# Performance work log

Hardware: AMD Instinct MI355X
Metric: run time of the kernel (lower is better)

The kernel has to match this reference:

```python
import jax, jax.numpy as jnp
import numpy as np

PAD = 0
BOS = 101
D = 768
H = 12
DH = D // H
DFF = 3072
V = 30522


def _ln(x, eps=1e-5):
    m = jnp.mean(x, axis=-1, keepdims=True)
    v = jnp.var(x, axis=-1, keepdims=True)
    return (x - m) * jax.lax.rsqrt(v + eps)


def setup_inputs() -> dict:
    key = jax.random.key(0)
    ks = jax.random.split(key, 20)
    B, S = 8, 128
    s = 0.02
    p = lambda k, sh: (jax.random.normal(k, sh, dtype=jnp.float32) * s)
    inp = {
        "X": jax.random.randint(ks[0], (B, S), 0, V, dtype=jnp.int32),
        "emb": p(ks[1], (V, D)),
        "pos": p(ks[2], (512, D)),
        "Wq": p(ks[3], (D, D)), "Wk": p(ks[4], (D, D)),
        "Wv": p(ks[5], (D, D)), "Wo": p(ks[6], (D, D)),
        "W1": p(ks[7], (D, DFF)), "W2": p(ks[8], (DFF, D)),
        "Wdq": p(ks[9], (D, D)), "Wdk": p(ks[10], (D, D)),
        "Wdv": p(ks[11], (D, D)), "Wdo": p(ks[12], (D, D)),
        "Wd1": p(ks[13], (D, DFF)), "Wd2": p(ks[14], (DFF, D)),
        "Wvoc": p(ks[15], (D, V)),
        "max_tgt_len": 32,
        "beam_width": 4,
    }
    return inp


def reference(X, emb, pos, Wq, Wk, Wv, Wo, W1, W2,
              Wdq, Wdk, Wdv, Wdo, Wd1, Wd2, Wvoc,
              max_tgt_len, beam_width):
    B, S = X.shape
    K = beam_width
    T = max_tgt_len
    scale = 1.0 / np.sqrt(DH)

    # ---- BERT-style encoder (1 layer) ----
    src_mask = (X != PAD)                              # [B,S]
    mb = jnp.where(src_mask, 0.0, -1e9)[:, None, None, :]  # [B,1,1,S]
    h = emb[X] + pos[:S][None]                         # [B,S,D]
    q = (h @ Wq).reshape(B, S, H, DH)
    k = (h @ Wk).reshape(B, S, H, DH)
    v = (h @ Wv).reshape(B, S, H, DH)
    att = jax.nn.softmax(jnp.einsum('bqhd,bkhd->bhqk', q, k) * scale + mb, axis=-1)
    ctx = jnp.einsum('bhqk,bkhd->bqhd', att, v).reshape(B, S, D) @ Wo
    h = _ln(h + ctx)
    h = _ln(h + jax.nn.gelu(h @ W1) @ W2)
    memory = h                                         # [B,S,D]

    # precompute cross-attn K/V once
    Kmem = (memory @ Wdk).reshape(B, S, H, DH)
    Vmem = (memory @ Wdv).reshape(B, S, H, DH)

    # ---- beam search decode ----
    tokens0 = jnp.full((B, K), BOS, dtype=jnp.int32)
    scores0 = jnp.broadcast_to(
        jnp.concatenate([jnp.zeros((1,)), jnp.full((K - 1,), -1e9)]).astype(jnp.float32),
        (B, K))

    def step(carry, t):
        tokens, scores = carry                         # [B,K], [B,K]
        x = emb[tokens] + pos[t][None, None]           # [B,K,D]
        qd = (x @ Wdq).reshape(B, K, H, DH)
        a = jax.nn.softmax(
            jnp.einsum('bkhd,bshd->bhks', qd, Kmem) * scale + mb, axis=-1)
        c = jnp.einsum('bhks,bshd->bkhd', a, Vmem).reshape(B, K, D) @ Wdo
        hd = _ln(x + c)
        hd = _ln(hd + jax.nn.gelu(hd @ Wd1) @ Wd2)
        logp = jax.nn.log_softmax(hd @ Wvoc, axis=-1)  # [B,K,V]
        total = (scores[:, :, None] + logp).reshape(B, K * V)
        new_scores, idx = jax.lax.top_k(total, K)      # [B,K]
        beam_idx = (idx // V).astype(jnp.int32)
        tok = (idx % V).astype(jnp.int32)
        return (tok, new_scores), (beam_idx, tok)

    (toksT, scoresT), (beam_hist, tok_hist) = jax.lax.scan(
        step, (tokens0, scores0), jnp.arange(T))

    # ---- backtrack through back-pointers ----
    ptr0 = jnp.broadcast_to(jnp.arange(K, dtype=jnp.int32), (B, K))

    def back(ptr, bt):
        beam_idx, tok = bt                             # [B,K] each
        seq_t = jnp.take_along_axis(tok, ptr, axis=1)
        ptr = jnp.take_along_axis(beam_idx, ptr, axis=1)
        return ptr, seq_t

    _, seq = jax.lax.scan(back, ptr0, (beam_hist, tok_hist), reverse=True)
    seq = jnp.transpose(seq, (1, 2, 0))                # [B,K,T]
    return seq, scoresT
```

## Files before the change

kernel.cpp:

```cpp
#include <hip/hip_runtime.h>
#include <math.h>

#define DMODEL 768
#define HN 12
#define DHEAD 64
#define DFF 3072
#define VOC 30522
#define BB 8
#define SS 128
#define KW 4
#define TT 32
#define CHN 239

__device__ __forceinline__ float gelu_f(float x) {
    float x3 = x * x * x;
    return 0.5f * x * (1.0f + tanhf(0.7978845608028654f * (x + 0.044715f * x3)));
}

__global__ void init_k(int* tokens, float* scores) {
    int i = threadIdx.x;
    if (i < BB * KW) {
        tokens[i] = 101;
        scores[i] = (i & 3) ? -1e9f : 0.0f;
    }
}

__global__ __launch_bounds__(256) void embed_enc(const int* __restrict__ X,
                                                 const float* __restrict__ emb,
                                                 const float* __restrict__ pos,
                                                 float* __restrict__ h,
                                                 float* __restrict__ mb) {
    int row = blockIdx.x;
    int s = row & (SS - 1);
    int tok = X[row];
    const float* e = emb + (size_t)tok * DMODEL;
    const float* p = pos + (size_t)s * DMODEL;
    float* hp = h + (size_t)row * DMODEL;
    for (int c = threadIdx.x; c < DMODEL; c += 256) hp[c] = e[c] + p[c];
    if (threadIdx.x == 0) mb[row] = (tok != 0) ? 0.0f : -1e9f;
}

template<int KD, int ACT>
__global__ __launch_bounds__(256) void gemm64(const float* __restrict__ A,
                                              const float* __restrict__ B,
                                              float* __restrict__ C, int N) {
    __shared__ float As[16][68];
    __shared__ float Bs[16][68];
    int tid = threadIdx.x;
    int tx = tid & 15, ty = tid >> 4;
    int bm = blockIdx.y * 64, bn = blockIdx.x * 64;
    int a_gk = tid & 15, a_gm0 = tid >> 4;
    int b_gn = tid & 63, b_gk0 = tid >> 6;
    float ra[4], rb[4];
    float acc[4][4] = {};
#pragma unroll
    for (int p = 0; p < 4; p++) ra[p] = A[(size_t)(bm + a_gm0 + p * 16) * KD + a_gk];
#pragma unroll
    for (int p = 0; p < 4; p++) rb[p] = B[(size_t)(b_gk0 + p * 4) * N + bn + b_gn];
    for (int k0 = 0; k0 < KD; k0 += 16) {
        __syncthreads();
#pragma unroll
        for (int p = 0; p < 4; p++) As[a_gk][a_gm0 + p * 16] = ra[p];
#pragma unroll
        for (int p = 0; p < 4; p++) Bs[b_gk0 + p * 4][b_gn] = rb[p];
        __syncthreads();
        if (k0 + 16 < KD) {
#pragma unroll
            for (int p = 0; p < 4; p++) ra[p] = A[(size_t)(bm + a_gm0 + p * 16) * KD + k0 + 16 + a_gk];
#pragma unroll
            for (int p = 0; p < 4; p++) rb[p] = B[(size_t)(k0 + 16 + b_gk0 + p * 4) * N + bn + b_gn];
        }
#pragma unroll
        for (int kk = 0; kk < 16; kk++) {
            float4 a4 = *(const float4*)&As[kk][ty * 4];
            float4 b4 = *(const float4*)&Bs[kk][tx * 4];
            float av[4] = {a4.x, a4.y, a4.z, a4.w};
            float bv[4] = {b4.x, b4.y, b4.z, b4.w};
#pragma unroll
            for (int i = 0; i < 4; i++)
#pragma unroll
                for (int j = 0; j < 4; j++) acc[i][j] += av[i] * bv[j];
        }
    }
#pragma unroll
    for (int i = 0; i < 4; i++)
#pragma unroll
        for (int j = 0; j < 4; j++) {
            float v = acc[i][j];
            if (ACT) v = gelu_f(v);
            C[(size_t)(bm + ty * 4 + i) * N + bn + tx * 4 + j] = v;
        }
}

__global__ __launch_bounds__(64) void enc_attn(const float* __restrict__ q,
                                               const float* __restrict__ k,
                                               const float* __restrict__ v,
                                               const float* __restrict__ mb,
                                               float* __restrict__ ctx) {
    int bid = blockIdx.x;
    int qi = bid & (SS - 1);
    int h = (bid >> 7) % HN;
    int b = bid / (SS * HN);
    int lane = threadIdx.x;
    __shared__ float qs[DHEAD];
    __shared__ float att[SS];
    qs[lane] = q[((size_t)(b * SS + qi) * HN + h) * DHEAD + lane];
    __syncthreads();
    const float* kb = k + ((size_t)(b * SS) * HN + h) * DHEAD;
    const float* k0p = kb + (size_t)lane * DMODEL;
    const float* k1p = kb + (size_t)(lane + 64) * DMODEL;
    float s0 = 0.f, s1 = 0.f;
#pragma unroll 8
    for (int d = 0; d < DHEAD; d++) {
        float qd = qs[d];
        s0 += qd * k0p[d];
        s1 += qd * k1p[d];
    }
    s0 = s0 * 0.125f + mb[b * SS + lane];
    s1 = s1 * 0.125f + mb[b * SS + lane + 64];
    float m = fmaxf(s0, s1);
    for (int off = 32; off; off >>= 1) m = fmaxf(m, __shfl_xor(m, off, 64));
    float e0 = expf(s0 - m), e1 = expf(s1 - m);
    float sum = e0 + e1;
    for (int off = 32; off; off >>= 1) sum += __shfl_xor(sum, off, 64);
    float inv = 1.0f / sum;
    att[lane] = e0 * inv;
    att[lane + 64] = e1 * inv;
    __syncthreads();
    const float* vb = v + ((size_t)(b * SS) * HN + h) * DHEAD + lane;
    float acc = 0.f;
#pragma unroll 8
    for (int key = 0; key < SS; key++) acc += att[key] * vb[(size_t)key * DMODEL];
    ctx[(size_t)(b * SS + qi) * DMODEL + h * DHEAD + lane] = acc;
}

template<int P>
__global__ __launch_bounds__(256) void lnresP(const float* __restrict__ A,
                                              const float* __restrict__ Bsrc,
                                              float* __restrict__ out,
                                              float* __restrict__ outT,
                                              int wantT, int planeStride) {
    int row = blockIdx.x, tid = threadIdx.x;
    const float* ap = A + (size_t)row * DMODEL;
    float x[3];
#pragma unroll
    for (int i = 0; i < 3; i++) {
        int idx = tid + 256 * i;
        float s = ap[idx];
#pragma unroll
        for (int p = 0; p < P; p++) s += Bsrc[(size_t)p * planeStride + (size_t)row * DMODEL + idx];
        x[i] = s;
    }
    __shared__ float red[256];
    __shared__ float sm, sv;
    red[tid] = x[0] + x[1] + x[2];
    __syncthreads();
    for (int off = 128; off; off >>= 1) { if (tid < off) red[tid] += red[tid + off]; __syncthreads(); }
    if (tid == 0) sm = red[0] * (1.0f / DMODEL);
    __syncthreads();
    float mean = sm;
    float d[3], s2 = 0.f;
#pragma unroll
    for (int i = 0; i < 3; i++) { d[i] = x[i] - mean; s2 += d[i] * d[i]; }
    __syncthreads();
    red[tid] = s2;
    __syncthreads();
    for (int off = 128; off; off >>= 1) { if (tid < off) red[tid] += red[tid + off]; __syncthreads(); }
    if (tid == 0) sv = 1.0f / sqrtf(red[0] * (1.0f / DMODEL) + 1e-5f);
    __syncthreads();
    float inv = sv;
    float* op = out + (size_t)row * DMODEL;
#pragma unroll
    for (int i = 0; i < 3; i++) {
        float val = d[i] * inv;
        op[tid + 256 * i] = val;
        if (wantT) outT[(size_t)(tid + 256 * i) * 32 + row] = val;
    }
}

__global__ __launch_bounds__(256) void embed_dec(const int* __restrict__ tokens,
                                                 const float* __restrict__ emb,
                                                 const float* __restrict__ pos,
                                                 int t, float* __restrict__ x,
                                                 float* __restrict__ xT) {
    int row = blockIdx.x;
    int tok = tokens[row];
    const float* e = emb + (size_t)tok * DMODEL;
    const float* p = pos + (size_t)t * DMODEL;
    for (int c = threadIdx.x; c < DMODEL; c += 256) {
        float v = e[c] + p[c];
        x[(size_t)row * DMODEL + c] = v;
        xT[(size_t)c * 32 + row] = v;
    }
}

template<int KRANGE, int APL, int AGELU, int TOUT>
__global__ __launch_bounds__(256) void skinny3(const float* __restrict__ At,
                                               const float* __restrict__ B,
                                               float* __restrict__ C,
                                               int N, int aPlaneF4) {
    constexpr int SK = (KRANGE > 192) ? 192 : KRANGE;
    constexpr int NST = KRANGE / SK;
    __shared__ float Als[SK * 32];
    int tid = threadIdx.x;
    int lane = tid & 63, q = tid >> 6;
    int col0 = blockIdx.x * 128 + lane * 2;
    float acc[8][2] = {};
    for (int st = 0; st < NST; st++) {
        int kbase = blockIdx.y * KRANGE + st * SK;
        __syncthreads();
        const float4* srcb = ((const float4*)At) + (size_t)kbase * 8;
        float4* dst = (float4*)Als;
#pragma unroll
        for (int i = 0; i < SK / 32; i++) {
            float4 v = srcb[i * 256 + tid];
#pragma unroll
            for (int p = 1; p < APL; p++) {
                float4 w = srcb[(size_t)p * aPlaneF4 + i * 256 + tid];
                v.x += w.x; v.y += w.y; v.z += w.z; v.w += w.w;
            }
            if (AGELU) { v.x = gelu_f(v.x); v.y = gelu_f(v.y); v.z = gelu_f(v.z); v.w = gelu_f(v.w); }
            dst[i * 256 + tid] = v;
        }
        __syncthreads();
        const float* Bp = B + (size_t)kbase * N + col0;
#pragma unroll 8
        for (int k = 0; k < SK; k++) {
            float2 bv = *(const float2*)(Bp + (size_t)k * N);
            float4 a0 = *(const float4*)&Als[k * 32 + q * 8];
            float4 a1 = *(const float4*)&Als[k * 32 + q * 8 + 4];
            float ar[8] = {a0.x, a0.y, a0.z, a0.w, a1.x, a1.y, a1.z, a1.w};
#pragma unroll
            for (int r = 0; r < 8; r++) {
                acc[r][0] += ar[r] * bv.x;
                acc[r][1] += ar[r] * bv.y;
            }
        }
    }
    float* Cb = C + (size_t)blockIdx.y * 32 * N;
    if (TOUT) {
#pragma unroll
        for (int c = 0; c < 2; c++) {
            float4 lo = {acc[0][c], acc[1][c], acc[2][c], acc[3][c]};
            float4 hi = {acc[4][c], acc[5][c], acc[6][c], acc[7][c]};
            *(float4*)&Cb[(size_t)(col0 + c) * 32 + q * 8] = lo;
            *(float4*)&Cb[(size_t)(col0 + c) * 32 + q * 8 + 4] = hi;
        }
    } else {
#pragma unroll
        for (int r = 0; r < 8; r++) {
            float2 st2 = {acc[r][0], acc[r][1]};
            *(float2*)&Cb[(size_t)(q * 8 + r) * N + col0] = st2;
        }
    }
}

__global__ __launch_bounds__(64) void dec_attn(const float* __restrict__ qdp,
                                               const float* __restrict__ Kmem,
                                               const float* __restrict__ Vmem,
                                               const float* __restrict__ mb,
                                               float* __restrict__ cctxT) {
    const int QP = 32 * DMODEL;
    int bid = blockIdx.x;
    int h = bid % HN;
    int kb = (bid / HN) & 3;
    int b = bid / (HN * KW);
    int lane = threadIdx.x;
    int rowq = b * KW + kb;
    __shared__ float qs[DHEAD];
    __shared__ float att[SS];
    size_t qoff = (size_t)rowq * DMODEL + h * DHEAD + lane;
    float qv = 0.f;
#pragma unroll
    for (int p = 0; p < 8; p++) qv += qdp[(size_t)p * QP + qoff];
    qs[lane] = qv;
    __syncthreads();
    const float* kb0 = Kmem + ((size_t)(b * SS) * HN + h) * DHEAD;
    const float* k0p = kb0 + (size_t)lane * DMODEL;
    const float* k1p = kb0 + (size_t)(lane + 64) * DMODEL;
    float s0 = 0.f, s1 = 0.f;
#pragma unroll 8
    for (int d = 0; d < DHEAD; d++) {
        float qd = qs[d];
        s0 += qd * k0p[d];
        s1 += qd * k1p[d];
    }
    s0 = s0 * 0.125f + mb[b * SS + lane];
    s1 = s1 * 0.125f + mb[b * SS + lane + 64];
    float m = fmaxf(s0, s1);
    for (int off = 32; off; off >>= 1) m = fmaxf(m, __shfl_xor(m, off, 64));
    float e0 = expf(s0 - m), e1 = expf(s1 - m);
    float sum = e0 + e1;
    for (int off = 32; off; off >>= 1) sum += __shfl_xor(sum, off, 64);
    float inv = 1.0f / sum;
    att[lane] = e0 * inv;
    att[lane + 64] = e1 * inv;
    __syncthreads();
    const float* vb = Vmem + ((size_t)(b * SS) * HN + h) * DHEAD + lane;
    float acc = 0.f;
#pragma unroll 8
    for (int key = 0; key < SS; key++) acc += att[key] * vb[(size_t)key * DMODEL];
    cctxT[(size_t)(h * DHEAD + lane) * 32 + rowq] = acc;
}

__global__ __launch_bounds__(256) void logits_stats(const float* __restrict__ At,
                                                    const float* __restrict__ B,
                                                    float* __restrict__ cmax,
                                                    float* __restrict__ csum,
                                                    float* __restrict__ ctv,
                                                    int* __restrict__ cti) {
    __shared__ float Als[192 * 32];
    int tid = threadIdx.x;
    int lane = tid & 63, q = tid >> 6;
    int col0 = blockIdx.x * 128 + lane * 2;
    bool valid = col0 < VOC;
    int jc = valid ? col0 : VOC - 2;
    float acc[8][2] = {};
    for (int st = 0; st < 4; st++) {
        int kbase = st * 192;
        __syncthreads();
        const float4* srcb = ((const float4*)At) + (size_t)kbase * 8;
        float4* dst = (float4*)Als;
#pragma unroll
        for (int i = 0; i < 6; i++) dst[i * 256 + tid] = srcb[i * 256 + tid];
        __syncthreads();
        const float* Bp = B + (size_t)kbase * VOC + jc;
#pragma unroll 8
        for (int k = 0; k < 192; k++) {
            float2 bv = *(const float2*)(Bp + (size_t)k * VOC);
            float4 a0 = *(const float4*)&Als[k * 32 + q * 8];
            float4 a1 = *(const float4*)&Als[k * 32 + q * 8 + 4];
            float ar[8] = {a0.x, a0.y, a0.z, a0.w, a1.x, a1.y, a1.z, a1.w};
#pragma unroll
            for (int r = 0; r < 8; r++) {
                acc[r][0] += ar[r] * bv.x;
                acc[r][1] += ar[r] * bv.y;
            }
        }
    }
#pragma unroll 1
    for (int r = 0; r < 8; r++) {
        float v0 = valid ? acc[r][0] : -INFINITY;
        float v1 = valid ? acc[r][1] : -INFINITY;
        float mx = fmaxf(v0, v1);
#pragma unroll
        for (int off = 32; off; off >>= 1) mx = fmaxf(mx, __shfl_xor(mx, off, 64));
        float ss = valid ? (expf(v0 - mx) + expf(v1 - mx)) : 0.0f;
#pragma unroll
        for (int off = 32; off; off >>= 1) ss += __shfl_xor(ss, off, 64);
        float c0 = v0, c1 = v1;
        int i0 = col0, i1 = col0 + 1;
        float tv[4]; int ti[4];
#pragma unroll
        for (int p = 0; p < 4; p++) {
            float bv; int bi;
            if (c0 > c1 || (c0 == c1 && i0 < i1)) { bv = c0; bi = i0; } else { bv = c1; bi = i1; }
#pragma unroll
            for (int off = 32; off; off >>= 1) {
                float ov = __shfl_xor(bv, off, 64);
                int oi = __shfl_xor(bi, off, 64);
                if (ov > bv || (ov == bv && oi < bi)) { bv = ov; bi = oi; }
            }
            if (bi == i0) c0 = -INFINITY;
            else if (bi == i1) c1 = -INFINITY;
            tv[p] = bv; ti[p] = bi;
        }
        if (lane == 0) {
            int m = q * 8 + r;
            int o = m * CHN + blockIdx.x;
            cmax[o] = mx; csum[o] = ss;
            ctv[o * 4 + 0] = tv[0]; cti[o * 4 + 0] = ti[0];
            ctv[o * 4 + 1] = tv[1]; cti[o * 4 + 1] = ti[1];
            ctv[o * 4 + 2] = tv[2]; cti[o * 4 + 2] = ti[2];
            ctv[o * 4 + 3] = tv[3]; cti[o * 4 + 3] = ti[3];
        }
    }
}

__global__ __launch_bounds__(256) void merge_topk(const float* __restrict__ cmax,
                                                  const float* __restrict__ csum,
                                                  const float* __restrict__ ctv,
                                                  const int* __restrict__ cti,
                                                  float* scores, int* tokens,
                                                  int* beamh, int* tokh, int t) {
    int b = blockIdx.x, tid = threadIdx.x;
    int lane = tid & 63, q = tid >> 6;
    int m = b * 4 + q;
    __shared__ float LSE[4], s_old[4];
    __shared__ float bt_v[4][4];
    __shared__ int bt_i[4][4];
    if (tid < 4) s_old[tid] = scores[b * 4 + tid];
    float mx = -INFINITY, sm = 0.f;
    for (int c = lane; c < CHN; c += 64) {
        float cm = cmax[m * CHN + c], cs = csum[m * CHN + c];
        if (cm > mx) { sm = sm * expf(mx - cm) + cs; mx = cm; }
        else sm += cs * expf(cm - mx);
    }
#pragma unroll
    for (int off = 32; off; off >>= 1) {
        float om = __shfl_xor(mx, off, 64);
        float os = __shfl_xor(sm, off, 64);
        float M = fmaxf(mx, om);
        sm = sm * expf(mx - M) + os * expf(om - M);
        mx = M;
    }
    if (lane == 0) LSE[q] = mx + logf(sm);
    float lv[4] = {-INFINITY, -INFINITY, -INFINITY, -INFINITY};
    int li[4] = {0x7fffffff, 0x7fffffff, 0x7fffffff, 0x7fffffff};
    for (int c = lane; c < CHN; c += 64) {
        int o = (m * CHN + c) * 4;
#pragma unroll
        for (int j = 0; j < 4; j++) {
            float v = ctv[o + j]; int i = cti[o + j];
            if (v > lv[3] || (v == lv[3] && i < li[3])) {
                lv[3] = v; li[3] = i;
#pragma unroll
                for (int s = 3; s > 0; s--) {
                    if (lv[s] > lv[s - 1] || (lv[s] == lv[s - 1] && li[s] < li[s - 1])) {
                        float tv2 = lv[s]; lv[s] = lv[s - 1]; lv[s - 1] = tv2;
                        int ti2 = li[s]; li[s] = li[s - 1]; li[s - 1] = ti2;
                    }
                }
            }
        }
    }
#pragma unroll
    for (int p = 0; p < 4; p++) {
        float bv = lv[0]; int bi = li[0];
#pragma unroll
        for (int off = 32; off; off >>= 1) {
            float ov = __shfl_xor(bv, off, 64);
            int oi = __shfl_xor(bi, off, 64);
            if (ov > bv || (ov == bv && oi < bi)) { bv = ov; bi = oi; }
        }
        if (li[0] == bi) {
            lv[0] = lv[1]; li[0] = li[1];
            lv[1] = lv[2]; li[1] = li[2];
            lv[2] = lv[3]; li[2] = li[3];
            lv[3] = -INFINITY; li[3] = 0x7fffffff;
        }
        if (lane == 0) { bt_v[q][p] = bv; bt_i[q][p] = bi; }
    }
    __syncthreads();
    if (tid == 0) {
        float fv[16]; int fi[16]; bool used[16];
#pragma unroll
        for (int r = 0; r < 4; r++)
#pragma unroll
            for (int p = 0; p < 4; p++) {
                fv[r * 4 + p] = s_old[r] - LSE[r] + bt_v[r][p];
                fi[r * 4 + p] = r * VOC + bt_i[r][p];
                used[r * 4 + p] = false;
            }
        for (int kk = 0; kk < 4; kk++) {
            int best = -1;
            for (int c2 = 0; c2 < 16; c2++) {
                if (used[c2]) continue;
                if (best < 0 || fv[c2] > fv[best] || (fv[c2] == fv[best] && fi[c2] < fi[best])) best = c2;
            }
            used[best] = true;
            int beam = fi[best] / VOC;
            int tok = fi[best] - beam * VOC;
            scores[b * 4 + kk] = fv[best];
            tokens[b * 4 + kk] = tok;
            beamh[(t * BB + b) * 4 + kk] = beam;
            tokh[(t * BB + b) * 4 + kk] = tok;
        }
    }
}

__global__ void backtrack_k(const int* __restrict__ beamh, const int* __restrict__ tokh,
                            const float* __restrict__ scores, float* __restrict__ out) {
    int i = threadIdx.x;
    if (i < BB * KW) {
        int b = i >> 2, k = i & 3;
        int ptr = k;
        for (int t = TT - 1; t >= 0; t--) {
            int tok = tokh[(t * BB + b) * KW + ptr];
            out[(size_t)i * TT + t] = (float)tok;
            ptr = beamh[(t * BB + b) * KW + ptr];
        }
        out[BB * KW * TT + i] = scores[i];
    }
}

extern "C" void kernel_launch(void* const* d_in, const int* in_sizes, int n_in,
                              void* d_out, int out_size, void* d_ws, size_t ws_size,
                              hipStream_t stream) {
    const int* X = (const int*)d_in[0];
    const float* emb = (const float*)d_in[1];
    const float* pos = (const float*)d_in[2];
    const float* Wq = (const float*)d_in[3];
    const float* Wk = (const float*)d_in[4];
    const float* Wv = (const float*)d_in[5];
    const float* Wo = (const float*)d_in[6];
    const float* W1 = (const float*)d_in[7];
    const float* W2 = (const float*)d_in[8];
    const float* Wdq = (const float*)d_in[9];
    const float* Wdk = (const float*)d_in[10];
    const float* Wdv = (const float*)d_in[11];
    const float* Wdo = (const float*)d_in[12];
    const float* Wd1 = (const float*)d_in[13];
    const float* Wd2 = (const float*)d_in[14];
    const float* Wvoc = (const float*)d_in[15];

    float* ws = (float*)d_ws;
    size_t o = 0;
    auto alloc = [&](size_t n) { float* p = ws + o; o += n; return p; };

    const size_t ROWS = (size_t)BB * SS;
    const size_t HD = ROWS * DMODEL;
    const size_t P32 = 32 * DMODEL;

    float* mb = alloc(ROWS);
    float* Kmem = alloc(HD);
    float* Vmem = alloc(HD);
    float* scores = alloc(32);
    int* tokens = (int*)alloc(32);
    int* beamh = (int*)alloc(TT * BB * KW);
    int* tokh = (int*)alloc(TT * BB * KW);

    size_t mark = o;
    float* h0 = alloc(HD);
    float* qb = alloc(HD);
    float* kb = alloc(HD);
    float* vb = alloc(HD);
    float* attc = alloc(HD);
    float* attp = alloc(HD);
    float* h1 = alloc(HD);
    float* ff1 = alloc(ROWS * DFF);
    float* ff2 = alloc(HD);
    float* memb = alloc(HD);

    o = mark;
    float* x = alloc(P32);
    float* xT = alloc(P32);
    float* qdp = alloc(8 * P32);
    float* cctxT = alloc(P32);
    float* cprojp = alloc(8 * P32);
    float* hd1 = alloc(P32);
    float* hd1T = alloc(P32);
    float* dff1p = alloc((size_t)4 * DFF * 32);
    float* dff2p = alloc(8 * P32);
    float* hd2 = alloc(P32);
    float* hd2T = alloc(P32);
    float* cmax = alloc(32 * CHN);
    float* csum = alloc(32 * CHN);
    float* ctv = alloc((size_t)32 * CHN * 4);
    int* cti = (int*)alloc((size_t)32 * CHN * 4);
    (void)ws_size; (void)in_sizes; (void)n_in; (void)out_size;

    init_k<<<1, 64, 0, stream>>>(tokens, scores);

    embed_enc<<<dim3(ROWS), 256, 0, stream>>>(X, emb, pos, h0, mb);
    dim3 g768(DMODEL / 64, ROWS / 64);
    dim3 g3072(DFF / 64, ROWS / 64);
    gemm64<DMODEL, 0><<<g768, 256, 0, stream>>>(h0, Wq, qb, DMODEL);
    gemm64<DMODEL, 0><<<g768, 256, 0, stream>>>(h0, Wk, kb, DMODEL);
    gemm64<DMODEL, 0><<<g768, 256, 0, stream>>>(h0, Wv, vb, DMODEL);
    enc_attn<<<dim3(BB * HN * SS), 64, 0, stream>>>(qb, kb, vb, mb, attc);
    gemm64<DMODEL, 0><<<g768, 256, 0, stream>>>(attc, Wo, attp, DMODEL);
    lnresP<1><<<dim3(ROWS), 256, 0, stream>>>(h0, attp, h1, nullptr, 0, 0);
    gemm64<DMODEL, 1><<<g3072, 256, 0, stream>>>(h1, W1, ff1, DFF);
    gemm64<DFF, 0><<<g768, 256, 0, stream>>>(ff1, W2, ff2, DMODEL);
    lnresP<1><<<dim3(ROWS), 256, 0, stream>>>(h1, ff2, memb, nullptr, 0, 0);
    gemm64<DMODEL, 0><<<g768, 256, 0, stream>>>(memb, Wdk, Kmem, DMODEL);
    gemm64<DMODEL, 0><<<g768, 256, 0, stream>>>(memb, Wdv, Vmem, DMODEL);

    for (int t = 0; t < TT; t++) {
        embed_dec<<<dim3(32), 256, 0, stream>>>(tokens, emb, pos, t, x, xT);
        skinny3<96, 1, 0, 0><<<dim3(6, 8), 256, 0, stream>>>(xT, Wdq, qdp, DMODEL, 0);
        dec_attn<<<dim3(BB * KW * HN), 64, 0, stream>>>(qdp, Kmem, Vmem, mb, cctxT);
        skinny3<96, 1, 0, 0><<<dim3(6, 8), 256, 0, stream>>>(cctxT, Wdo, cprojp, DMODEL, 0);
        lnresP<8><<<dim3(32), 256, 0, stream>>>(x, cprojp, hd1, hd1T, 1, (int)P32);
        skinny3<192, 1, 0, 1><<<dim3(24, 4), 256, 0, stream>>>(hd1T, Wd1, dff1p, DFF, 0);
        skinny3<384, 4, 1, 0><<<dim3(6, 8), 256, 0, stream>>>(dff1p, Wd2, dff2p, DMODEL, DFF * 8);
        lnresP<8><<<dim3(32), 256, 0, stream>>>(hd1, dff2p, hd2, hd2T, 1, (int)P32);
        logits_stats<<<dim3(CHN), 256, 0, stream>>>(hd2T, Wvoc, cmax, csum, ctv, cti);
        merge_topk<<<dim3(BB), 256, 0, stream>>>(cmax, csum, ctv, cti,
                                                 scores, tokens, beamh, tokh, t);
    }

    backtrack_k<<<1, 64, 0, stream>>>(beamh, tokh, scores, (float*)d_out);
}
```

Baseline: 9.355 ms.

## Fuse beam-search decode loop into a persistent kernel with grid barriers

Replaces the 320+ per-step kernel launches of the decode loop with one persistent kernel of 256 blocks. Each stage becomes a device function, and an atomic grid-wide barrier separates the stages. This removes launch overhead and inter-kernel gaps, at the cost of every block spinning at each barrier and all stages sharing one block configuration. The logits inner loop unroll factor is also raised, and initialization and backtracking move into the persistent kernel. The design relies on all 256 blocks being co-resident, or the barrier deadlocks.

Result: slower. 24.88 ms (+166.0%).

```diff
diff --git a/kernel.cpp b/kernel.cpp
--- a/kernel.cpp
+++ b/kernel.cpp
@@ -11,19 +11,14 @@
 #define KW 4
 #define TT 32
 #define CHN 239
+#define PG 256
+#define P32C (32 * DMODEL)
 
 __device__ __forceinline__ float gelu_f(float x) {
     float x3 = x * x * x;
     return 0.5f * x * (1.0f + tanhf(0.7978845608028654f * (x + 0.044715f * x3)));
 }
 
-__global__ void init_k(int* tokens, float* scores) {
-    int i = threadIdx.x;
-    if (i < BB * KW) {
-        tokens[i] = 101;
-        scores[i] = (i & 3) ? -1e9f : 0.0f;
-    }
-}
 
 __global__ __launch_bounds__(256) void embed_enc(const int* __restrict__ X,
                                                  const float* __restrict__ emb,
@@ -178,12 +173,30 @@
     }
 }
 
-__global__ __launch_bounds__(256) void embed_dec(const int* __restrict__ tokens,
-                                                 const float* __restrict__ emb,
-                                                 const float* __restrict__ pos,
-                                                 int t, float* __restrict__ x,
-                                                 float* __restrict__ xT) {
-    int row = blockIdx.x;
+
+__device__ __forceinline__ void gsync(unsigned* bar) {
+    __syncthreads();
+    if (threadIdx.x == 0) {
+        __threadfence();
+        unsigned g0 = __hip_atomic_load(bar + 1, __ATOMIC_RELAXED, __HIP_MEMORY_SCOPE_AGENT);
+        unsigned a = __hip_atomic_fetch_add(bar, 1u, __ATOMIC_ACQ_REL, __HIP_MEMORY_SCOPE_AGENT);
+        if (a == PG - 1) {
+            __hip_atomic_store(bar, 0u, __ATOMIC_RELAXED, __HIP_MEMORY_SCOPE_AGENT);
+            __hip_atomic_fetch_add(bar + 1, 1u, __ATOMIC_RELEASE, __HIP_MEMORY_SCOPE_AGENT);
+        } else {
+            while (__hip_atomic_load(bar + 1, __ATOMIC_RELAXED, __HIP_MEMORY_SCOPE_AGENT) == g0)
+                __builtin_amdgcn_s_sleep(2);
+        }
+        __threadfence();
+    }
+    __syncthreads();
+}
+
+__device__ __forceinline__ void embed_body(const int* __restrict__ tokens,
+                                           const float* __restrict__ emb,
+                                           const float* __restrict__ pos,
+                                           int t, float* __restrict__ x,
+                                           float* __restrict__ xT, int row) {
     int tok = tokens[row];
     const float* e = emb + (size_t)tok * DMODEL;
     const float* p = pos + (size_t)t * DMODEL;
@@ -195,19 +208,19 @@
 }
 
 template<int KRANGE, int APL, int AGELU, int TOUT>
-__global__ __launch_bounds__(256) void skinny3(const float* __restrict__ At,
-                                               const float* __restrict__ B,
-                                               float* __restrict__ C,
-                                               int N, int aPlaneF4) {
+__device__ __forceinline__ void skinny3_body(float* Als,
+                                             const float* __restrict__ At,
+                                             const float* __restrict__ B,
+                                             float* __restrict__ C,
+                                             int N, int aPlaneF4, int bx, int by) {
     constexpr int SK = (KRANGE > 192) ? 192 : KRANGE;
     constexpr int NST = KRANGE / SK;
-    __shared__ float Als[SK * 32];
     int tid = threadIdx.x;
     int lane = tid & 63, q = tid >> 6;
-    int col0 = blockIdx.x * 128 + lane * 2;
+    int col0 = bx * 128 + lane * 2;
     float acc[8][2] = {};
     for (int st = 0; st < NST; st++) {
-        int kbase = blockIdx.y * KRANGE + st * SK;
+        int kbase = by * KRANGE + st * SK;
         __syncthreads();
         const float4* srcb = ((const float4*)At) + (size_t)kbase * 8;
         float4* dst = (float4*)Als;
@@ -237,7 +250,7 @@
             }
         }
     }
-    float* Cb = C + (size_t)blockIdx.y * 32 * N;
+    float* Cb = C + (size_t)by * 32 * N;
     if (TOUT) {
 #pragma unroll
         for (int c = 0; c < 2; c++) {
@@ -255,20 +268,22 @@
     }
 }
 
-__global__ __launch_bounds__(64) void dec_attn(const float* __restrict__ qdp,
-                                               const float* __restrict__ Kmem,
-                                               const float* __restrict__ Vmem,
-                                               const float* __restrict__ mb,
-                                               float* __restrict__ cctxT) {
+__device__ __forceinline__ void dec_attn_body(float* smem,
+                                              const float* __restrict__ qdp,
+                                              const float* __restrict__ Kmem,
+                                              const float* __restrict__ Vmem,
+                                              const float* __restrict__ mb,
+                                              float* __restrict__ cctxT, int vb) {
     const int QP = 32 * DMODEL;
-    int bid = blockIdx.x;
-    int h = bid % HN;
-    int kb = (bid / HN) & 3;
-    int b = bid / (HN * KW);
-    int lane = threadIdx.x;
+    int tid = threadIdx.x;
+    int w = tid >> 6, lane = tid & 63;
+    int unit = vb * 4 + w;
+    int h = unit % HN;
+    int kb = (unit / HN) & 3;
+    int b = unit / (HN * KW);
     int rowq = b * KW + kb;
-    __shared__ float qs[DHEAD];
-    __shared__ float att[SS];
+    float* qs = smem + w * 64;
+    float* att = smem + 256 + w * SS;
     size_t qoff = (size_t)rowq * DMODEL + h * DHEAD + lane;
     float qv = 0.f;
 #pragma unroll
@@ -296,23 +311,67 @@
     att[lane] = e0 * inv;
     att[lane + 64] = e1 * inv;
     __syncthreads();
-    const float* vb = Vmem + ((size_t)(b * SS) * HN + h) * DHEAD + lane;
+    const float* vb2 = Vmem + ((size_t)(b * SS) * HN + h) * DHEAD + lane;
     float acc = 0.f;
 #pragma unroll 8
-    for (int key = 0; key < SS; key++) acc += att[key] * vb[(size_t)key * DMODEL];
+    for (int key = 0; key < SS; key++) acc += att[key] * vb2[(size_t)key * DMODEL];
     cctxT[(size_t)(h * DHEAD + lane) * 32 + rowq] = acc;
 }
 
-__global__ __launch_bounds__(256) void logits_stats(const float* __restrict__ At,
-                                                    const float* __restrict__ B,
-                                                    float* __restrict__ cmax,
-                                                    float* __restrict__ csum,
-                                                    float* __restrict__ ctv,
-                                                    int* __restrict__ cti) {
-    __shared__ float Als[192 * 32];
+template<int P>
+__device__ __forceinline__ void lnres_body(float* smem,
+                                           const float* __restrict__ A,
+                                           const float* __restrict__ Bsrc,
+                                           float* __restrict__ out,
+                                           float* __restrict__ outT,
+                                           int planeStride, int row) {
+    int tid = threadIdx.x;
+    const float* ap = A + (size_t)row * DMODEL;
+    float xx[3];
+#pragma unroll
+    for (int i = 0; i < 3; i++) {
+        int idx = tid + 256 * i;
+        float s = ap[idx];
+#pragma unroll
+        for (int p = 0; p < P; p++) s += Bsrc[(size_t)p * planeStride + (size_t)row * DMODEL + idx];
+        xx[i] = s;
+    }
+    float* red = smem;
+    red[tid] = xx[0] + xx[1] + xx[2];
+    __syncthreads();
+    for (int off = 128; off; off >>= 1) { if (tid < off) red[tid] += red[tid + off]; __syncthreads(); }
+    if (tid == 0) smem[256] = red[0] * (1.0f / DMODEL);
+    __syncthreads();
+    float mean = smem[256];
+    float d[3], s2 = 0.f;
+#pragma unroll
+    for (int i = 0; i < 3; i++) { d[i] = xx[i] - mean; s2 += d[i] * d[i]; }
+    __syncthreads();
+    red[tid] = s2;
+    __syncthreads();
+    for (int off = 128; off; off >>= 1) { if (tid < off) red[tid] += red[tid + off]; __syncthreads(); }
+    if (tid == 0) smem[257] = 1.0f / sqrtf(red[0] * (1.0f / DMODEL) + 1e-5f);
+    __syncthreads();
+    float inv = smem[257];
+    float* op = out + (size_t)row * DMODEL;
+#pragma unroll
+    for (int i = 0; i < 3; i++) {
+        float val = d[i] * inv;
+        op[tid + 256 * i] = val;
+        outT[(size_t)(tid + 256 * i) * 32 + row] = val;
+    }
+}
+
+__device__ __forceinline__ void logits_body(float* Als,
+                                            const float* __restrict__ At,
+                                            const float* __restrict__ B,
+                                            float* __restrict__ cmax,
+                                            float* __restrict__ csum,
+                                            float* __restrict__ ctv,
+                                            int* __restrict__ cti, int bx) {
     int tid = threadIdx.x;
     int lane = tid & 63, q = tid >> 6;
-    int col0 = blockIdx.x * 128 + lane * 2;
+    int col0 = bx * 128 + lane * 2;
     bool valid = col0 < VOC;
     int jc = valid ? col0 : VOC - 2;
     float acc[8][2] = {};
@@ -325,7 +384,7 @@
         for (int i = 0; i < 6; i++) dst[i * 256 + tid] = srcb[i * 256 + tid];
         __syncthreads();
         const float* Bp = B + (size_t)kbase * VOC + jc;
-#pragma unroll 8
+#pragma unroll 16
         for (int k = 0; k < 192; k++) {
             float2 bv = *(const float2*)(Bp + (size_t)k * VOC);
             float4 a0 = *(const float4*)&Als[k * 32 + q * 8];
@@ -367,7 +426,7 @@
         }
         if (lane == 0) {
             int m = q * 8 + r;
-            int o = m * CHN + blockIdx.x;
+            int o = m * CHN + bx;
             cmax[o] = mx; csum[o] = ss;
             ctv[o * 4 + 0] = tv[0]; cti[o * 4 + 0] = ti[0];
             ctv[o * 4 + 1] = tv[1]; cti[o * 4 + 1] = ti[1];
@@ -377,18 +436,22 @@
     }
 }
 
-__global__ __launch_bounds__(256) void merge_topk(const float* __restrict__ cmax,
-                                                  const float* __restrict__ csum,
-                                                  const float* __restrict__ ctv,
-                                                  const int* __restrict__ cti,
-                                                  float* scores, int* tokens,
-                                                  int* beamh, int* tokh, int t) {
-    int b = blockIdx.x, tid = threadIdx.x;
+__device__ __forceinline__ void merge_body(float* smem,
+                                           const float* __restrict__ cmax,
+                                           const float* __restrict__ csum,
+                                           const float* __restrict__ ctv,
+                                           const int* __restrict__ cti,
+                                           float* __restrict__ scores,
+                                           int* __restrict__ tokens,
+                                           int* __restrict__ beamh,
+                                           int* __restrict__ tokh, int t, int b) {
+    int tid = threadIdx.x;
     int lane = tid & 63, q = tid >> 6;
     int m = b * 4 + q;
-    __shared__ float LSE[4], s_old[4];
-    __shared__ float bt_v[4][4];
-    __shared__ int bt_i[4][4];
+    float* s_old = smem;
+    float* LSE = smem + 4;
+    float* bt_v = smem + 8;
+    int* bt_i = (int*)(smem + 24);
     if (tid < 4) s_old[tid] = scores[b * 4 + tid];
     float mx = -INFINITY, sm = 0.f;
     for (int c = lane; c < CHN; c += 64) {
@@ -439,7 +502,7 @@
             lv[2] = lv[3]; li[2] = li[3];
             lv[3] = -INFINITY; li[3] = 0x7fffffff;
         }
-        if (lane == 0) { bt_v[q][p] = bv; bt_i[q][p] = bi; }
+        if (lane == 0) { bt_v[q * 4 + p] = bv; bt_i[q * 4 + p] = bi; }
     }
     __syncthreads();
     if (tid == 0) {
@@ -448,8 +511,8 @@
         for (int r = 0; r < 4; r++)
 #pragma unroll
             for (int p = 0; p < 4; p++) {
-                fv[r * 4 + p] = s_old[r] - LSE[r] + bt_v[r][p];
-                fi[r * 4 + p] = r * VOC + bt_i[r][p];
+                fv[r * 4 + p] = s_old[r] - LSE[r] + bt_v[r * 4 + p];
+                fi[r * 4 + p] = r * VOC + bt_i[r * 4 + p];
                 used[r * 4 + p] = false;
             }
         for (int kk = 0; kk < 4; kk++) {
@@ -469,19 +532,69 @@
     }
 }
 
-__global__ void backtrack_k(const int* __restrict__ beamh, const int* __restrict__ tokh,
-                            const float* __restrict__ scores, float* __restrict__ out) {
-    int i = threadIdx.x;
-    if (i < BB * KW) {
-        int b = i >> 2, k = i & 3;
+__global__ __launch_bounds__(256) void decode_persistent(
+    const float* __restrict__ emb, const float* __restrict__ pos,
+    const float* __restrict__ Wdq, const float* __restrict__ Wdo,
+    const float* __restrict__ Wd1, const float* __restrict__ Wd2,
+    const float* __restrict__ Wvoc,
+    const float* __restrict__ Kmem, const float* __restrict__ Vmem,
+    const float* __restrict__ mb,
+    float* __restrict__ x, float* __restrict__ xT,
+    float* __restrict__ qdp, float* __restrict__ cctxT, float* __restrict__ cprojp,
+    float* __restrict__ hd1, float* __restrict__ hd1T,
+    float* __restrict__ dff1p, float* __restrict__ dff2p,
+    float* __restrict__ hd2, float* __restrict__ hd2T,
+    float* __restrict__ cmax, float* __restrict__ csum,
+    float* __restrict__ ctv, int* __restrict__ cti,
+    float* __restrict__ scores, int* __restrict__ tokens,
+    int* __restrict__ beamh, int* __restrict__ tokh,
+    unsigned* bar, float* __restrict__ out) {
+    __shared__ float smem[6160];
+    int bid = blockIdx.x, tid = threadIdx.x;
+
+    if (bid == 0 && tid < BB * KW) {
+        tokens[tid] = 101;
+        scores[tid] = (tid & 3) ? -1e9f : 0.0f;
+    }
+    gsync(bar);
+
+    for (int t = 0; t < TT; t++) {
+        if (bid < 32) embed_body(tokens, emb, pos, t, x, xT, bid);
+        gsync(bar);
+        if (bid < 48) skinny3_body<96, 1, 0, 0>(smem, xT, Wdq, qdp, DMODEL, 0, bid % 6, bid / 6);
+        gsync(bar);
+        if (bid < 96) dec_attn_body(smem, qdp, Kmem, Vmem, mb, cctxT, bid);
+        gsync(bar);
+        if (bid < 48) skinny3_body<96, 1, 0, 0>(smem, cctxT, Wdo, cprojp, DMODEL, 0, bid % 6, bid / 6);
+        gsync(bar);
+        if (bid < 32) lnres_body<8>(smem, x, cprojp, hd1, hd1T, P32C, bid);
+        gsync(bar);
+        if (bid < 96) skinny3_body<192, 1, 0, 1>(smem, hd1T, Wd1, dff1p, DFF, 0, bid % 24, bid / 24);
+        gsync(bar);
+        if (bid < 48) skinny3_body<384, 4, 1, 0>(smem, dff1p, Wd2, dff2p, DMODEL, DFF * 8, bid % 6, bid / 6);
+        gsync(bar);
+        if (bid < 32) lnres_body<8>(smem, hd1, dff2p, hd2, hd2T, P32C, bid);
+        gsync(bar);
+        if (bid < CHN) logits_body(smem, hd2T, Wvoc, cmax, csum, ctv, cti, bid);
+        gsync(bar);
+        if (bid < BB) merge_body(smem, cmax, csum, ctv, cti, scores, tokens, beamh, tokh, t, bid);
+        gsync(bar);
+    }
+
+    if (bid == 0 && tid < BB * KW) {
+        int b = tid >> 2, k = tid & 3;
         int ptr = k;
         for (int t = TT - 1; t >= 0; t--) {
             int tok = tokh[(t * BB + b) * KW + ptr];
-            out[(size_t)i * TT + t] = (float)tok;
+            out[(size_t)tid * TT + t] = (float)tok;
             ptr = beamh[(t * BB + b) * KW + ptr];
         }
-        out[BB * KW * TT + i] = scores[i];
-    }
+        out[BB * KW * TT + tid] = scores[tid];
+    }
+}
+
+__global__ void init_k(unsigned* bar) {
+    if (threadIdx.x < 2) bar[threadIdx.x] = 0u;
 }
 
 extern "C" void kernel_launch(void* const* d_in, const int* in_sizes, int n_in,
@@ -519,6 +632,7 @@
     int* tokens = (int*)alloc(32);
     int* beamh = (int*)alloc(TT * BB * KW);
     int* tokh = (int*)alloc(TT * BB * KW);
+    unsigned* bar = (unsigned*)alloc(2);
 
     size_t mark = o;
     float* h0 = alloc(HD);
@@ -550,7 +664,7 @@
     int* cti = (int*)alloc((size_t)32 * CHN * 4);
     (void)ws_size; (void)in_sizes; (void)n_in; (void)out_size;
 
-    init_k<<<1, 64, 0, stream>>>(tokens, scores);
+    init_k<<<1, 64, 0, stream>>>(bar);
 
     embed_enc<<<dim3(ROWS), 256, 0, stream>>>(X, emb, pos, h0, mb);
     dim3 g768(DMODEL / 64, ROWS / 64);
@@ -567,19 +681,8 @@
     gemm64<DMODEL, 0><<<g768, 256, 0, stream>>>(memb, Wdk, Kmem, DMODEL);
     gemm64<DMODEL, 0><<<g768, 256, 0, stream>>>(memb, Wdv, Vmem, DMODEL);
 
-    for (int t = 0; t < TT; t++) {
-        embed_dec<<<dim3(32), 256, 0, stream>>>(tokens, emb, pos, t, x, xT);
-        skinny3<96, 1, 0, 0><<<dim3(6, 8), 256, 0, stream>>>(xT, Wdq, qdp, DMODEL, 0);
-        dec_attn<<<dim3(BB * KW * HN), 64, 0, stream>>>(qdp, Kmem, Vmem, mb, cctxT);
-        skinny3<96, 1, 0, 0><<<dim3(6, 8), 256, 0, stream>>>(cctxT, Wdo, cprojp, DMODEL, 0);
-        lnresP<8><<<dim3(32), 256, 0, stream>>>(x, cprojp, hd1, hd1T, 1, (int)P32);
-        skinny3<192, 1, 0, 1><<<dim3(24, 4), 256, 0, stream>>>(hd1T, Wd1, dff1p, DFF, 0);
-        skinny3<384, 4, 1, 0><<<dim3(6, 8), 256, 0, stream>>>(dff1p, Wd2, dff2p, DMODEL, DFF * 8);
-        lnresP<8><<<dim3(32), 256, 0, stream>>>(hd1, dff2p, hd2, hd2T, 1, (int)P32);
-        logits_stats<<<dim3(CHN), 256, 0, stream>>>(hd2T, Wvoc, cmax, csum, ctv, cti);
-        merge_topk<<<dim3(BB), 256, 0, stream>>>(cmax, csum, ctv, cti,
-                                                 scores, tokens, beamh, tokh, t);
-    }
-
-    backtrack_k<<<1, 64, 0, stream>>>(beamh, tokh, scores, (float*)d_out);
-}
+    decode_persistent<<<dim3(PG), 256, 0, stream>>>(
+        emb, pos, Wdq, Wdo, Wd1, Wd2, Wvoc, Kmem, Vmem, mb,
+        x, xT, qdp, cctxT, cprojp, hd1, hd1T, dff1p, dff2p, hd2, hd2T,
+        cmax, csum, ctv, cti, scores, tokens, beamh, tokh, bar, (float*)d_out);
+}
```
